# Optimization experiments

Measured on AMD Instinct MI355X. Metric: run time of the kernel, lower is better.

## Reference

```python
import jax, jax.numpy as jnp
import numpy as np

NUM_NODES = 200000
MEM_DIM = 128
TIME_DIM = 100
EDGE_DIM = 128
MSG_DIM = 256
E = 65536


def setup_inputs() -> dict:
    key = jax.random.key(0)
    ks = jax.random.split(key, 12)
    basis_freq = jnp.asarray(1.0 / 10 ** np.linspace(0, 9, TIME_DIM), dtype=jnp.float32)
    return {
        "src": jax.random.randint(ks[0], (E,), 0, NUM_NODES),
        "dst": jax.random.randint(ks[1], (E,), 0, NUM_NODES),
        "ts": jax.random.uniform(ks[2], (E,), dtype=jnp.float32),
        "edge_feats": jax.random.normal(ks[3], (E, EDGE_DIM), dtype=jnp.float32),
        "memory": jax.random.normal(ks[4], (NUM_NODES, MEM_DIM), dtype=jnp.float32),
        "last_update_ts": jnp.zeros((NUM_NODES,), dtype=jnp.float32),
        "basis_freq": basis_freq,
        "phase": jnp.zeros((TIME_DIM,), dtype=jnp.float32),
        "W_msg": jax.random.normal(ks[5], (MSG_DIM, 2 * MEM_DIM + TIME_DIM + EDGE_DIM), dtype=jnp.float32) * 0.05,
        "b_msg": jnp.zeros((MSG_DIM,), dtype=jnp.float32),
        "W_ih": jax.random.normal(ks[6], (3 * MEM_DIM, MSG_DIM), dtype=jnp.float32) * 0.05,
        "W_hh": jax.random.normal(ks[7], (3 * MEM_DIM, MEM_DIM), dtype=jnp.float32) * 0.05,
        "b_ih": jnp.zeros((3 * MEM_DIM,), dtype=jnp.float32),
        "b_hh": jnp.zeros((3 * MEM_DIM,), dtype=jnp.float32),
    }


def _time_enc(dt, basis_freq, phase):
    # dt: [E,1] -> [E,TIME_DIM]
    return jnp.cos(dt * basis_freq[None, :] + phase[None, :])


def reference(src, dst, ts, edge_feats, memory, last_update_ts,
              basis_freq, phase, W_msg, b_msg, W_ih, W_hh, b_ih, b_hh):
    n = memory.shape[0]
    ts_col = ts[:, None]                               # [E,1]
    prev_src_mem = memory[src]                         # [E,D]
    prev_dst_mem = memory[dst]
    tenc_src = _time_enc(ts_col - last_update_ts[src][:, None], basis_freq, phase)
    tenc_dst = _time_enc(ts_col - last_update_ts[dst][:, None], basis_freq, phase)

    # message MLP (dropout = identity, eval mode)
    x_dst = jnp.concatenate([prev_src_mem, prev_dst_mem, tenc_dst, edge_feats], axis=1)
    x_src = jnp.concatenate([prev_dst_mem, prev_src_mem, tenc_src, edge_feats], axis=1)
    msg_dst = jax.nn.relu(x_dst @ W_msg.T + b_msg)     # [E,M]
    msg_src = jax.nn.relu(x_src @ W_msg.T + b_msg)

    all_nodes = jnp.concatenate([src, dst], axis=0)    # [2E]
    all_msgs = jnp.concatenate([msg_src, msg_dst], axis=0)  # [2E,M]

    # per-node mean aggregation via segment sums (vectorized unique-loop)
    msg_sum = jax.ops.segment_sum(all_msgs, all_nodes, num_segments=n)
    counts = jax.ops.segment_sum(jnp.ones_like(all_nodes, dtype=msg_sum.dtype),
                                 all_nodes, num_segments=n)
    agg = msg_sum / jnp.maximum(counts, 1.0)[:, None]  # [N,M]

    # GRU cell update (torch.nn.GRUCell semantics)
    gi = agg @ W_ih.T + b_ih                           # [N,3D]
    gh = memory @ W_hh.T + b_hh
    i_r, i_z, i_n = jnp.split(gi, 3, axis=1)
    h_r, h_z, h_n = jnp.split(gh, 3, axis=1)
    r = jax.nn.sigmoid(i_r + h_r)
    z = jax.nn.sigmoid(i_z + h_z)
    nn_ = jnp.tanh(i_n + r * h_n)
    h_new = (1.0 - z) * nn_ + z * memory

    updated = counts > 0
    new_memory = jnp.where(updated[:, None], h_new, memory)

    # last_update_ts scatter-amax
    ts_rep = jnp.concatenate([ts, ts], axis=0)
    max_ts = jnp.zeros((n,), dtype=last_update_ts.dtype).at[all_nodes].max(ts_rep)
    new_last_update_ts = jnp.maximum(last_update_ts, max_ts)
    return new_memory, new_last_update_ts
```

## Files before the change

### kernel.cpp

```cpp
#include <hip/hip_runtime.h>
#include <hip/hip_bf16.h>
#include <math.h>

#define NNODES 200000
#define EDGES  65536
#define NSIDES (2*EDGES)
#define MD 128
#define TD 100
#define EDIM 128
#define MSGD 256
#define KX 512
#define KG 384
#define NSCAN 782
#define GBLK 64

typedef __attribute__((ext_vector_type(8))) short bf16x8;
typedef __attribute__((ext_vector_type(4))) float f32x4;

#define O_COUNTS    0u
#define O_NUMUPD    800000u
#define O_BSUMC     800004u
#define O_BSUMF     803132u
#define O_UPDLIST   806272u
#define O_SEGSTART  1330592u
#define O_CNTLIST   1854912u
#define O_BMSG      2379200u
#define O_BG        2641344u
#define O_BH        2936256u
#define O_MSGBUF    2969088u
#define O_UPDFLAG   (2969088u + 67108864u)
#define WS_NEEDED   (2969088ull + 67108864ull + 200000ull)

__device__ __forceinline__ short f2bf(float v) {
    unsigned x = __float_as_uint(v);
    unsigned r = (x + 0x7fffu + ((x >> 16) & 1u)) >> 16;
    return (short)r;
}
__device__ __forceinline__ unsigned pk2bf(float a, float b) {
    unsigned xa = __float_as_uint(a);
    unsigned xb = __float_as_uint(b);
    unsigned ra = (xa + 0x7fffu + ((xa >> 16) & 1u)) >> 16;
    unsigned rb = (xb + 0x7fffu + ((xb >> 16) & 1u)) & 0xffff0000u;
    return ra | rb;
}
__device__ __forceinline__ float bflo(unsigned u) { return __uint_as_float(u << 16); }
__device__ __forceinline__ float bfhi(unsigned u) { return __uint_as_float(u & 0xffff0000u); }
__device__ __forceinline__ float bf2f(unsigned short u) {
    return __uint_as_float(((unsigned)u) << 16);
}
__device__ __forceinline__ f32x4 mfma16(bf16x8 a, bf16x8 b, f32x4 c) {
    return __builtin_amdgcn_mfma_f32_16x16x32_bf16(a, b, c, 0, 0, 0);
}

__global__ __launch_bounds__(256) void k_copy_ts(const float* __restrict__ last,
                                                 float* __restrict__ out_ts) {
    int i = blockIdx.x * 256 + threadIdx.x;
    if (i < NNODES / 4) ((float4*)out_ts)[i] = ((const float4*)last)[i];
}

__global__ __launch_bounds__(256) void k_copy_mem(const float* __restrict__ mem,
                                                  const unsigned char* __restrict__ updflag,
                                                  float* __restrict__ out) {
    size_t idx = (size_t)blockIdx.x * 256 + threadIdx.x;
    if (idx >= (size_t)NNODES * 32) return;
    int node = (int)(idx >> 5);
    if (updflag[node]) return;
    ((float4*)out)[idx] = ((const float4*)mem)[idx];
}

__global__ __launch_bounds__(256) void k_pack(const float* __restrict__ wmsg,
                                              const float* __restrict__ wih,
                                              const float* __restrict__ whh,
                                              short* __restrict__ bmsgp,
                                              short* __restrict__ bgp,
                                              short* __restrict__ bhp) {
    const int NM = 16 * 16 * 64 * 8;
    const int NG = 12 * 24 * 64 * 8;
    const int NH = 4 * 8 * 64 * 8;
    int idx = blockIdx.x * 256 + threadIdx.x;
    if (idx < NM) {
        int j = idx & 7, l = (idx >> 3) & 63, nf = (idx >> 9) & 15, ks = idx >> 13;
        int n = nf * 16 + (l & 15);
        int k = ks * 32 + ((l >> 4) << 3) + j;
        bmsgp[idx] = f2bf(k < 484 ? wmsg[n * 484 + k] : 0.f);
    } else if (idx < NM + NG) {
        int i = idx - NM;
        int j = i & 7, l = (i >> 3) & 63, rest = i >> 9;
        int nf = rest % 24, ks = rest / 24;
        int n = nf * 16 + (l & 15);
        int k = ks * 32 + ((l >> 4) << 3) + j;
        float v = (k < 256) ? wih[n * 256 + k] : whh[n * 128 + (k - 256)];
        bgp[i] = f2bf(v);
    } else if (idx < NM + NG + NH) {
        int i = idx - NM - NG;
        int j = i & 7, l = (i >> 3) & 63, rest = i >> 9;
        int nf = rest & 7, ks = rest >> 3;
        int n = 256 + nf * 16 + (l & 15);
        int k = ks * 32 + ((l >> 4) << 3) + j;
        bhp[i] = f2bf(whh[n * 128 + k]);
    }
}

__global__ __launch_bounds__(256) void k_edges(const int* __restrict__ src, const int* __restrict__ dst,
                                               const float* __restrict__ ts,
                                               int* __restrict__ counts, float* __restrict__ out_ts) {
    int e = blockIdx.x * blockDim.x + threadIdx.x;
    if (e >= EDGES) return;
    int s = src[e], d = dst[e];
    unsigned tb = __float_as_uint(ts[e]);
    atomicAdd(&counts[s], 1);
    atomicAdd(&counts[d], 1);
    atomicMax((unsigned*)&out_ts[s], tb);
    atomicMax((unsigned*)&out_ts[d], tb);
}

__global__ __launch_bounds__(256) void k_scan1(const int* __restrict__ counts,
                                               int* __restrict__ bsumC, int* __restrict__ bsumF) {
    __shared__ int sC[256], sF[256];
    int t = threadIdx.x, i = blockIdx.x * 256 + t;
    int c = (i < NNODES) ? counts[i] : 0;
    sC[t] = c; sF[t] = (c > 0) ? 1 : 0;
    __syncthreads();
    for (int off = 128; off > 0; off >>= 1) {
        if (t < off) { sC[t] += sC[t + off]; sF[t] += sF[t + off]; }
        __syncthreads();
    }
    if (t == 0) { bsumC[blockIdx.x] = sC[0]; bsumF[blockIdx.x] = sF[0]; }
}

__global__ __launch_bounds__(1024) void k_scan2(int* __restrict__ bsumC, int* __restrict__ bsumF,
                                                int* __restrict__ numupd) {
    __shared__ int sC[1024], sF[1024];
    int t = threadIdx.x;
    int c = (t < NSCAN) ? bsumC[t] : 0;
    int f = (t < NSCAN) ? bsumF[t] : 0;
    sC[t] = c; sF[t] = f;
    __syncthreads();
    for (int off = 1; off < 1024; off <<= 1) {
        int vc = (t >= off) ? sC[t - off] : 0;
        int vf = (t >= off) ? sF[t - off] : 0;
        __syncthreads();
        sC[t] += vc; sF[t] += vf;
        __syncthreads();
    }
    if (t < NSCAN) { bsumC[t] = sC[t] - c; bsumF[t] = sF[t] - f; }
    if (t == 0) numupd[0] = sF[1023];
}

__global__ __launch_bounds__(256) void k_scan3(int* __restrict__ counts,
                                               const int* __restrict__ bsumC, const int* __restrict__ bsumF,
                                               int* __restrict__ updlist, int* __restrict__ segstart,
                                               int* __restrict__ cntlist, const int* __restrict__ numupd,
                                               unsigned char* __restrict__ updflag) {
    __shared__ int sC[256], sF[256];
    int t = threadIdx.x, b = blockIdx.x, i = b * 256 + t;
    int c = (i < NNODES) ? counts[i] : 0;
    int fl = (c > 0) ? 1 : 0;
    sC[t] = c; sF[t] = fl;
    __syncthreads();
    for (int off = 1; off < 256; off <<= 1) {
        int vc = (t >= off) ? sC[t - off] : 0;
        int vf = (t >= off) ? sF[t - off] : 0;
        __syncthreads();
        sC[t] += vc; sF[t] += vf;
        __syncthreads();
    }
    if (i < NNODES) {
        int segC = bsumC[b] + sC[t] - c;
        int rank = bsumF[b] + sF[t] - fl;
        if (fl) {
            updlist[rank]  = i;
            segstart[rank] = segC;
            cntlist[rank]  = c;
        }
        updflag[i] = (unsigned char)fl;
        counts[i] = segC;
        if (i == NNODES - 1) segstart[numupd[0]] = segC + c;
    }
}

__global__ __launch_bounds__(512) void k_msg(const int* __restrict__ src, const int* __restrict__ dst,
                                             const float* __restrict__ ts, const float* __restrict__ ef,
                                             const float* __restrict__ mem, const float* __restrict__ last,
                                             const float* __restrict__ bfq, const float* __restrict__ ph,
                                             const short* __restrict__ Bp, const float* __restrict__ bmsg,
                                             int* __restrict__ cursor, unsigned short* __restrict__ msgbuf) {
    __shared__ short As[64 * KX];
    __shared__ int srcS[32], dstS[32], posS[64];
    __shared__ float dtS[64];
    const int t = threadIdx.x;
    const int e0 = blockIdx.x * 32;

    if (t < 64) {
        int el = t >> 1, which = t & 1;
        int e = e0 + el;
        int s = src[e], d = dst[e];
        int self = which ? d : s;
        if (which == 0) { srcS[el] = s; dstS[el] = d; }
        dtS[t]  = ts[e] - last[self];
        posS[t] = atomicAdd(&cursor[self], 1);
    }
    __syncthreads();

    const int c4 = t & 31;
    const int rg = t >> 5;
    #pragma unroll
    for (int i = 0; i < 4; ++i) {
        int nr = rg + i * 16;
        int el = nr >> 1, which = nr & 1;
        int node = which ? dstS[el] : srcS[el];
        float4 v = *(const float4*)&mem[(size_t)node * MD + c4 * 4];
        uint2 b = make_uint2(pk2bf(v.x, v.y), pk2bf(v.z, v.w));
        int rA = 2 * el, rB = 2 * el + 1;
        int swA = (rA & 7) << 3, swB = (rB & 7) << 3;
        int c16 = c4 * 4;
        if (which == 0) {
            *(uint2*)&As[rA * KX + ((128 + c16) ^ swA)] = b;
            *(uint2*)&As[rB * KX + ((0   + c16) ^ swB)] = b;
        } else {
            *(uint2*)&As[rA * KX + ((0   + c16) ^ swA)] = b;
            *(uint2*)&As[rB * KX + ((128 + c16) ^ swB)] = b;
        }
    }
    #pragma unroll
    for (int i = 0; i < 2; ++i) {
        int el = rg + i * 16;
        float4 v = *(const float4*)&ef[(size_t)(e0 + el) * EDIM + c4 * 4];
        uint2 b = make_uint2(pk2bf(v.x, v.y), pk2bf(v.z, v.w));
        int k = 356 + c4 * 4;
        int rA = 2 * el, rB = 2 * el + 1;
        *(uint2*)&As[rA * KX + (k ^ ((rA & 7) << 3))] = b;
        *(uint2*)&As[rB * KX + (k ^ ((rB & 7) << 3))] = b;
    }
    {
        int s = t & 63, jg = t >> 6;
        float dt = dtS[s];
        int sw = (s & 7) << 3;
        int j1 = min(jg * 13 + 13, TD);
        for (int j = jg * 13; j < j1; ++j) {
            float v = __cosf(fmaf(dt, bfq[j], ph[j]));
            As[s * KX + ((256 + j) ^ sw)] = f2bf(v);
        }
    }
    if (t < 448) {
        int s = t / 7, p = t % 7;
        int sw = (s & 7) << 3;
        int k = 484 + p * 4;
        *(short4*)&As[s * KX + (k ^ sw)] = make_short4(0, 0, 0, 0);
    }
    __syncthreads();

    const int w = t >> 6, l = t & 63, lc = l & 15, lq = l >> 4;
    f32x4 acc[4][2];
    #pragma unroll
    for (int i = 0; i < 4; ++i)
        #pragma unroll
        for (int j = 0; j < 2; ++j) acc[i][j] = (f32x4){0.f, 0.f, 0.f, 0.f};

    const int rsw = (lc & 7) << 3;
    for (int ks = 0; ks < 16; ++ks) {
        bf16x8 a[4];
        #pragma unroll
        for (int rt = 0; rt < 4; ++rt)
            a[rt] = *(const bf16x8*)&As[(rt * 16 + lc) * KX + ((ks * 32 + (lq << 3)) ^ rsw)];
        #pragma unroll
        for (int f = 0; f < 2; ++f) {
            bf16x8 b = *(const bf16x8*)(Bp + (size_t)(ks * 16 + w * 2 + f) * 512 + l * 8);
            #pragma unroll
            for (int rt = 0; rt < 4; ++rt)
                acc[rt][f] = mfma16(a[rt], b, acc[rt][f]);
        }
    }

    float bb[2];
    #pragma unroll
    for (int f = 0; f < 2; ++f) bb[f] = bmsg[w * 32 + f * 16 + lc];
    #pragma unroll
    for (int rt = 0; rt < 4; ++rt) {
        #pragma unroll
        for (int jj = 0; jj < 4; ++jj) {
            int srow = rt * 16 + lq * 4 + jj;
            unsigned short* orow = msgbuf + (size_t)posS[srow] * MSGD;
            #pragma unroll
            for (int f = 0; f < 2; ++f) {
                int c = w * 32 + f * 16 + lc;
                float v = fmaxf(acc[rt][f][jj] + bb[f], 0.f);
                orow[c] = (unsigned short)f2bf(v);
            }
        }
    }
}

__global__ __launch_bounds__(512) void k_gru(const int* __restrict__ updlist, const int* __restrict__ segstart,
                                             const int* __restrict__ cntlist, const int* __restrict__ numupd,
                                             const unsigned short* __restrict__ msgbuf,
                                             const float* __restrict__ mem,
                                             const short* __restrict__ Bg, const short* __restrict__ Bh,
                                             const float* __restrict__ bih, const float* __restrict__ bhh,
                                             float* __restrict__ outmem) {
    __shared__ short Ag[GBLK * KG];
    __shared__ int sb[GBLK + 1];
    __shared__ int nodesh[GBLK];
    __shared__ float invh[GBLK];
    const int nu = *numupd;
    const int slot0 = blockIdx.x * GBLK;
    if (slot0 >= nu) return;
    const int t = threadIdx.x;
    if (t < GBLK + 1) sb[t] = segstart[min(slot0 + t, nu)];
    if (t < GBLK) {
        int slot = slot0 + t;
        if (slot < nu) { nodesh[t] = updlist[slot]; invh[t] = 1.f / (float)cntlist[slot]; }
        else           { nodesh[t] = -1;            invh[t] = 0.f; }
    }
    __syncthreads();

    {
        const int c4 = t & 31, rg = t >> 5;
        #pragma unroll
        for (int i = 0; i < 4; ++i) {
            int s = rg + i * 16;
            int node = nodesh[s];
            float4 v = make_float4(0.f, 0.f, 0.f, 0.f);
            if (node >= 0) v = *(const float4*)&mem[(size_t)node * MD + c4 * 4];
            int sw = (s & 7) << 3;
            *(uint2*)&Ag[s * KG + ((256 + c4 * 4) ^ sw)] =
                make_uint2(pk2bf(v.x, v.y), pk2bf(v.z, v.w));
        }
    }
    {
        const int g = t >> 3, q = t & 7;
        float acc[32];
        #pragma unroll
        for (int m = 0; m < 32; ++m) acc[m] = 0.f;
        const int j0 = sb[g], j1 = sb[g + 1];
        for (int j = j0; j < j1; ++j) {
            const unsigned short* rp = msgbuf + (size_t)j * MSGD + q * 32;
            #pragma unroll
            for (int h = 0; h < 4; ++h) {
                uint4 u = *(const uint4*)(rp + h * 8);
                acc[h*8+0] += bflo(u.x); acc[h*8+1] += bfhi(u.x);
                acc[h*8+2] += bflo(u.y); acc[h*8+3] += bfhi(u.y);
                acc[h*8+4] += bflo(u.z); acc[h*8+5] += bfhi(u.z);
                acc[h*8+6] += bflo(u.w); acc[h*8+7] += bfhi(u.w);
            }
        }
        const float inv = invh[g];
        const int sw = (g & 7) << 3;
        #pragma unroll
        for (int h = 0; h < 4; ++h) {
            uint4 o;
            o.x = pk2bf(acc[h*8+0] * inv, acc[h*8+1] * inv);
            o.y = pk2bf(acc[h*8+2] * inv, acc[h*8+3] * inv);
            o.z = pk2bf(acc[h*8+4] * inv, acc[h*8+5] * inv);
            o.w = pk2bf(acc[h*8+6] * inv, acc[h*8+7] * inv);
            *(uint4*)&Ag[g * KG + ((q * 32 + h * 8) ^ sw)] = o;
        }
    }
    __syncthreads();

    const int w = t >> 6, l = t & 63, lc = l & 15, lq = l >> 4;
    f32x4 accS[4][3], accH[4];
    #pragma unroll
    for (int rt = 0; rt < 4; ++rt) {
        #pragma unroll
        for (int g = 0; g < 3; ++g) accS[rt][g] = (f32x4){0.f, 0.f, 0.f, 0.f};
        accH[rt] = (f32x4){0.f, 0.f, 0.f, 0.f};
    }

    const int rsw = (lc & 7) << 3;
    for (int ks = 0; ks < 12; ++ks) {
        bf16x8 a[4];
        #pragma unroll
        for (int rt = 0; rt < 4; ++rt)
            a[rt] = *(const bf16x8*)&Ag[(rt * 16 + lc) * KG + ((ks * 32 + (lq << 3)) ^ rsw)];
        #pragma unroll
        for (int g = 0; g < 3; ++g) {
            bf16x8 b = *(const bf16x8*)(Bg + (size_t)(ks * 24 + g * 8 + w) * 512 + l * 8);
            #pragma unroll
            for (int rt = 0; rt < 4; ++rt)
                accS[rt][g] = mfma16(a[rt], b, accS[rt][g]);
        }
        if (ks >= 8) {
            bf16x8 b = *(const bf16x8*)(Bh + (size_t)((ks - 8) * 8 + w) * 512 + l * 8);
            #pragma unroll
            for (int rt = 0; rt < 4; ++rt)
                accH[rt] = mfma16(a[rt], b, accH[rt]);
        }
    }

    {
        int d = w * 16 + lc;
        float br  = bih[d] + bhh[d];
        float bz  = bih[MD + d] + bhh[MD + d];
        float bin = bih[2 * MD + d];
        float bhn = bhh[2 * MD + d];
        #pragma unroll
        for (int rt = 0; rt < 4; ++rt) {
            #pragma unroll
            for (int jj = 0; jj < 4; ++jj) {
                int srow = rt * 16 + lq * 4 + jj;
                int node = nodesh[srow];
                if (node < 0) continue;
                float S_r = accS[rt][0][jj] + br;
                float S_z = accS[rt][1][jj] + bz;
                float hn  = accH[rt][jj] + bhn;
                float in_ = accS[rt][2][jj] - accH[rt][jj] + bin;
                float rr = 1.f / (1.f + __expf(-S_r));
                float zz = 1.f / (1.f + __expf(-S_z));
                float x  = fminf(fmaxf(in_ + rr * hn, -15.f), 15.f);
                float ex = __expf(-2.f * x);
                float nn = (1.f - ex) / (1.f + ex);
                int sw = (srow & 7) << 3;
                float mv = bf2f((unsigned short)Ag[srow * KG + ((256 + d) ^ sw)]);
                outmem[(size_t)node * MD + d] = (1.f - zz) * nn + zz * mv;
            }
        }
    }
}

extern "C" void kernel_launch(void* const* d_in, const int* in_sizes, int n_in,
                              void* d_out, int out_size, void* d_ws, size_t ws_size,
                              hipStream_t stream) {
    const int*   src  = (const int*)d_in[0];
    const int*   dst  = (const int*)d_in[1];
    const float* ts   = (const float*)d_in[2];
    const float* ef   = (const float*)d_in[3];
    const float* mem  = (const float*)d_in[4];
    const float* last = (const float*)d_in[5];
    const float* bfq  = (const float*)d_in[6];
    const float* ph   = (const float*)d_in[7];
    const float* wmsg = (const float*)d_in[8];
    const float* bmsg = (const float*)d_in[9];
    const float* wih  = (const float*)d_in[10];
    const float* whh  = (const float*)d_in[11];
    const float* bih  = (const float*)d_in[12];
    const float* bhh  = (const float*)d_in[13];
    float* out = (float*)d_out;
    char* ws = (char*)d_ws;

    if (ws_size < WS_NEEDED) return;

    int* counts   = (int*)(ws + O_COUNTS);
    int* numupd   = (int*)(ws + O_NUMUPD);
    int* bsumC    = (int*)(ws + O_BSUMC);
    int* bsumF    = (int*)(ws + O_BSUMF);
    int* updlist  = (int*)(ws + O_UPDLIST);
    int* segstart = (int*)(ws + O_SEGSTART);
    int* cntlist  = (int*)(ws + O_CNTLIST);
    short* bmsgp  = (short*)(ws + O_BMSG);
    short* bgp    = (short*)(ws + O_BG);
    short* bhp    = (short*)(ws + O_BH);
    unsigned short* msgbuf = (unsigned short*)(ws + O_MSGBUF);
    unsigned char*  updflag = (unsigned char*)(ws + O_UPDFLAG);
    float* out_ts = out + (size_t)NNODES * MD;

    hipMemsetAsync(ws + O_COUNTS, 0, 800004, stream);

    k_copy_ts<<<(NNODES / 4 + 255) / 256, 256, 0, stream>>>(last, out_ts);
    k_pack <<<1152, 256, 0, stream>>>(wmsg, wih, whh, bmsgp, bgp, bhp);
    k_edges<<<EDGES / 256, 256, 0, stream>>>(src, dst, ts, counts, out_ts);
    k_scan1<<<NSCAN, 256, 0, stream>>>(counts, bsumC, bsumF);
    k_scan2<<<1, 1024, 0, stream>>>(bsumC, bsumF, numupd);
    k_scan3<<<NSCAN, 256, 0, stream>>>(counts, bsumC, bsumF, updlist, segstart, cntlist, numupd, updflag);
    k_copy_mem<<<(NNODES * 32 + 255) / 256, 256, 0, stream>>>(mem, updflag, out);
    k_msg  <<<EDGES / 32, 512, 0, stream>>>(src, dst, ts, ef, mem, last, bfq, ph, bmsgp, bmsg, counts, msgbuf);
    k_gru  <<<NSIDES / GBLK, 512, 0, stream>>>(updlist, segstart, cntlist, numupd, msgbuf, mem, bgp, bhp, bih, bhh, out);
}
```

Measured before the change: 195.9 us.

## Fold copy kernels into pack and msg launches; stage GRU output through LDS

The last_update_ts copy is folded into the k_pack launch as extra blocks, and the masked memory copy is folded into k_msg as extra blocks, which removes two kernel launches and lets the copy run alongside the message GEMM. The GRU epilogue now writes results into a swizzled LDS tile and then stores whole 512-byte rows with float4 writes, replacing scattered 4-byte stores. The cost is extra barriers and LDS reuse in k_gru, and heavier launches for k_msg, whose large LDS footprint may limit how many copy blocks can be resident at once.

```diff
diff --git a/kernel.cpp b/kernel.cpp
--- a/kernel.cpp
+++ b/kernel.cpp
@@ -13,6 +13,10 @@
 #define KG 384
 #define NSCAN 782
 #define GBLK 64
+#define MSGBLKS (EDGES/32)
+#define CPBLKS  6250
+#define PACKBLKS 1152
+#define TSBLKS   196
 
 typedef __attribute__((ext_vector_type(8))) short bf16x8;
 typedef __attribute__((ext_vector_type(4))) float f32x4;
@@ -52,28 +56,19 @@
     return __builtin_amdgcn_mfma_f32_16x16x32_bf16(a, b, c, 0, 0, 0);
 }
 
-__global__ __launch_bounds__(256) void k_copy_ts(const float* __restrict__ last,
-                                                 float* __restrict__ out_ts) {
-    int i = blockIdx.x * 256 + threadIdx.x;
-    if (i < NNODES / 4) ((float4*)out_ts)[i] = ((const float4*)last)[i];
-}
-
-__global__ __launch_bounds__(256) void k_copy_mem(const float* __restrict__ mem,
-                                                  const unsigned char* __restrict__ updflag,
-                                                  float* __restrict__ out) {
-    size_t idx = (size_t)blockIdx.x * 256 + threadIdx.x;
-    if (idx >= (size_t)NNODES * 32) return;
-    int node = (int)(idx >> 5);
-    if (updflag[node]) return;
-    ((float4*)out)[idx] = ((const float4*)mem)[idx];
-}
-
 __global__ __launch_bounds__(256) void k_pack(const float* __restrict__ wmsg,
                                               const float* __restrict__ wih,
                                               const float* __restrict__ whh,
                                               short* __restrict__ bmsgp,
                                               short* __restrict__ bgp,
-                                              short* __restrict__ bhp) {
+                                              short* __restrict__ bhp,
+                                              const float* __restrict__ last,
+                                              float* __restrict__ out_ts) {
+    if (blockIdx.x >= PACKBLKS) {
+        int i = (blockIdx.x - PACKBLKS) * 256 + threadIdx.x;
+        if (i < NNODES / 4) ((float4*)out_ts)[i] = ((const float4*)last)[i];
+        return;
+    }
     const int NM = 16 * 16 * 64 * 8;
     const int NG = 12 * 24 * 64 * 8;
     const int NH = 4 * 8 * 64 * 8;
@@ -184,11 +179,24 @@
                                              const float* __restrict__ mem, const float* __restrict__ last,
                                              const float* __restrict__ bfq, const float* __restrict__ ph,
                                              const short* __restrict__ Bp, const float* __restrict__ bmsg,
-                                             int* __restrict__ cursor, unsigned short* __restrict__ msgbuf) {
+                                             int* __restrict__ cursor, unsigned short* __restrict__ msgbuf,
+                                             const unsigned char* __restrict__ updflag,
+                                             float* __restrict__ outmem) {
     __shared__ short As[64 * KX];
     __shared__ int srcS[32], dstS[32], posS[64];
     __shared__ float dtS[64];
     const int t = threadIdx.x;
+
+    if (blockIdx.x >= MSGBLKS) {
+        size_t base = (size_t)(blockIdx.x - MSGBLKS) * 1024 + t * 2;
+        #pragma unroll
+        for (int i = 0; i < 2; ++i) {
+            size_t idx = base + i;
+            int node = (int)(idx >> 5);
+            if (!updflag[node]) ((float4*)outmem)[idx] = ((const float4*)mem)[idx];
+        }
+        return;
+    }
     const int e0 = blockIdx.x * 32;
 
     if (t < 64) {
@@ -388,7 +396,22 @@
         }
     }
 
+    float mvr[4][4];
     {
+        int d = w * 16 + lc;
+        #pragma unroll
+        for (int rt = 0; rt < 4; ++rt)
+            #pragma unroll
+            for (int jj = 0; jj < 4; ++jj) {
+                int srow = rt * 16 + lq * 4 + jj;
+                int sw = (srow & 7) << 3;
+                mvr[rt][jj] = bf2f((unsigned short)Ag[srow * KG + ((256 + d) ^ sw)]);
+            }
+    }
+    __syncthreads();
+
+    {
+        float* O = (float*)Ag;
         int d = w * 16 + lc;
         float br  = bih[d] + bhh[d];
         float bz  = bih[MD + d] + bhh[MD + d];
@@ -399,8 +422,6 @@
             #pragma unroll
             for (int jj = 0; jj < 4; ++jj) {
                 int srow = rt * 16 + lq * 4 + jj;
-                int node = nodesh[srow];
-                if (node < 0) continue;
                 float S_r = accS[rt][0][jj] + br;
                 float S_z = accS[rt][1][jj] + bz;
                 float hn  = accH[rt][jj] + bhn;
@@ -410,9 +431,25 @@
                 float x  = fminf(fmaxf(in_ + rr * hn, -15.f), 15.f);
                 float ex = __expf(-2.f * x);
                 float nn = (1.f - ex) / (1.f + ex);
-                int sw = (srow & 7) << 3;
-                float mv = bf2f((unsigned short)Ag[srow * KG + ((256 + d) ^ sw)]);
-                outmem[(size_t)node * MD + d] = (1.f - zz) * nn + zz * mv;
+                float outv = (1.f - zz) * nn + zz * mvr[rt][jj];
+                O[srow * 128 + (d ^ ((srow & 7) << 2))] = outv;
+            }
+        }
+    }
+    __syncthreads();
+
+    {
+        const float* O = (const float*)Ag;
+        int row = t >> 3, q = t & 7;
+        int node = nodesh[row];
+        if (node >= 0) {
+            float* orow = outmem + (size_t)node * MD;
+            int sw2 = (row & 7) << 2;
+            #pragma unroll
+            for (int i = 0; i < 4; ++i) {
+                int c0 = (q * 4 + i) * 4;
+                float4 v = *(const float4*)&O[row * 128 + (c0 ^ sw2)];
+                *(float4*)&orow[c0] = v;
             }
         }
     }
@@ -456,13 +493,12 @@
 
     hipMemsetAsync(ws + O_COUNTS, 0, 800004, stream);
 
-    k_copy_ts<<<(NNODES / 4 + 255) / 256, 256, 0, stream>>>(last, out_ts);
-    k_pack <<<1152, 256, 0, stream>>>(wmsg, wih, whh, bmsgp, bgp, bhp);
+    k_pack <<<PACKBLKS + TSBLKS, 256, 0, stream>>>(wmsg, wih, whh, bmsgp, bgp, bhp, last, out_ts);
     k_edges<<<EDGES / 256, 256, 0, stream>>>(src, dst, ts, counts, out_ts);
     k_scan1<<<NSCAN, 256, 0, stream>>>(counts, bsumC, bsumF);
     k_scan2<<<1, 1024, 0, stream>>>(bsumC, bsumF, numupd);
     k_scan3<<<NSCAN, 256, 0, stream>>>(counts, bsumC, bsumF, updlist, segstart, cntlist, numupd, updflag);
-    k_copy_mem<<<(NNODES * 32 + 255) / 256, 256, 0, stream>>>(mem, updflag, out);
-    k_msg  <<<EDGES / 32, 512, 0, stream>>>(src, dst, ts, ef, mem, last, bfq, ph, bmsgp, bmsg, counts, msgbuf);
+    k_msg  <<<MSGBLKS + CPBLKS, 512, 0, stream>>>(src, dst, ts, ef, mem, last, bfq, ph, bmsgp, bmsg,
+                                                  counts, msgbuf, updflag, out);
     k_gru  <<<NSIDES / GBLK, 512, 0, stream>>>(updlist, segstart, cntlist, numupd, msgbuf, mem, bgp, bhp, bih, bhh, out);
 }
```

After: 242.6 us. 1.24x slower.
